# Kernel optimization log

Hardware: AMD Instinct MI355X
Metric: run time of the kernel (lower is better)

Reference implementation:

```python
import jax, jax.numpy as jnp
import numpy as np

EPS = 1e-5
K = 3
N_TAP = K * K


def _bn(x, g, b, m, v):
    # eval-mode batchnorm over channel axis 1 of NCHW
    inv = g / jnp.sqrt(v + EPS)
    return x * inv[None, :, None, None] + (b - m * inv)[None, :, None, None]


def _silu(x):
    return x * jax.nn.sigmoid(x)


def _dcn(x, offset, mask, w, b, pad=1):
    """Modulated deformable conv (DCNv2), stride 1.
    x: [B,C,H,W], offset: [B,2n,H,W] ((dy,dx) per tap), mask: [B,n,H,W],
    w: [O,C,K,K], b: [O]."""
    B, C, H, W = x.shape
    O = w.shape[0]
    ky, kx = jnp.meshgrid(jnp.arange(K), jnp.arange(K), indexing='ij')
    ky = ky.reshape(N_TAP).astype(x.dtype)
    kx = kx.reshape(N_TAP).astype(x.dtype)
    off = offset.reshape(B, N_TAP, 2, H, W)
    base_y = jnp.arange(H, dtype=x.dtype)[None, None, :, None]
    base_x = jnp.arange(W, dtype=x.dtype)[None, None, None, :]
    # fractional sample positions [B,n,H,W]
    py = base_y - pad + ky[None, :, None, None] + off[:, :, 0]
    px = base_x - pad + kx[None, :, None, None] + off[:, :, 1]
    y0 = jnp.floor(py)
    x0 = jnp.floor(px)
    fy = py - y0
    fx = px - x0
    y0i = y0.astype(jnp.int32)
    x0i = x0.astype(jnp.int32)
    x_flat = x.reshape(B, C, 1, H * W)

    def corner(yi, xi, wgt):
        valid = (yi >= 0) & (yi < H) & (xi >= 0) & (xi < W)
        idx = (jnp.clip(yi, 0, H - 1) * W + jnp.clip(xi, 0, W - 1)).reshape(B, 1, N_TAP, H * W)
        v = jnp.take_along_axis(x_flat, idx, axis=-1)  # [B,C,n,HW]
        return v * (wgt * valid.astype(x.dtype)).reshape(B, 1, N_TAP, H * W)

    acc = corner(y0i, x0i, (1 - fy) * (1 - fx))
    acc = acc + corner(y0i, x0i + 1, (1 - fy) * fx)
    acc = acc + corner(y0i + 1, x0i, fy * (1 - fx))
    acc = acc + corner(y0i + 1, x0i + 1, fy * fx)
    val = acc.reshape(B, C, N_TAP, H, W) * mask[:, None]  # modulation
    out = jnp.einsum('bcnhw,ocn->bohw', val, w.reshape(O, C, N_TAP))
    return out + b[None, :, None, None]


def setup_inputs() -> dict:
    key = jax.random.key(0)
    ks = jax.random.split(key, 16)
    B, C1, H, W = 8, 256, 80, 80
    C2 = 256
    Ch = 128  # c_ = int(c2 * 0.5)
    d = {}
    d['x'] = jax.random.normal(ks[0], (B, C1, H, W), jnp.float32)
    # cv1: 1x1 conv (no bias) + BN
    d['cv1_w'] = jax.random.normal(ks[1], (Ch, C1), jnp.float32) * (1.0 / np.sqrt(C1))
    d['bn1_g'] = jax.random.uniform(ks[2], (Ch,), jnp.float32, 0.5, 1.5)
    d['bn1_b'] = jax.random.normal(ks[3], (Ch,), jnp.float32) * 0.1
    d['bn1_m'] = jax.random.normal(ks[4], (Ch,), jnp.float32) * 0.1
    d['bn1_v'] = jax.random.uniform(ks[5], (Ch,), jnp.float32, 0.5, 1.5)
    # offset/mask predictor 3x3 conv (small weights -> modest deformation)
    d['off_w'] = jax.random.normal(ks[6], (3 * N_TAP, Ch, K, K), jnp.float32) * 0.01
    d['off_b'] = jnp.zeros((3 * N_TAP,), jnp.float32)
    # dcn main weight/bias
    d['dcn_w'] = jax.random.normal(ks[7], (Ch, Ch, K, K), jnp.float32) * (1.0 / np.sqrt(Ch * N_TAP))
    d['dcn_b'] = jnp.zeros((Ch,), jnp.float32)
    d['bn2_g'] = jax.random.uniform(ks[8], (Ch,), jnp.float32, 0.5, 1.5)
    d['bn2_b'] = jax.random.normal(ks[9], (Ch,), jnp.float32) * 0.1
    d['bn2_m'] = jax.random.normal(ks[10], (Ch,), jnp.float32) * 0.1
    d['bn2_v'] = jax.random.uniform(ks[11], (Ch,), jnp.float32, 0.5, 1.5)
    # cv2: 1x1 conv (no bias) + BN
    d['cv2_w'] = jax.random.normal(ks[12], (C2, Ch), jnp.float32) * (1.0 / np.sqrt(Ch))
    d['bn3_g'] = jax.random.uniform(ks[13], (C2,), jnp.float32, 0.5, 1.5)
    d['bn3_b'] = jax.random.normal(ks[14], (C2,), jnp.float32) * 0.1
    d['bn3_m'] = jax.random.normal(ks[15], (C2,), jnp.float32) * 0.1
    d['bn3_v'] = jnp.ones((C2,), jnp.float32)
    return d


def reference(x, cv1_w, bn1_g, bn1_b, bn1_m, bn1_v,
              off_w, off_b, dcn_w, dcn_b, bn2_g, bn2_b, bn2_m, bn2_v,
              cv2_w, bn3_g, bn3_b, bn3_m, bn3_v):
    # cv1: 1x1 conv -> BN -> SiLU
    y = _silu(_bn(jnp.einsum('bchw,oc->bohw', x, cv1_w), bn1_g, bn1_b, bn1_m, bn1_v))
    # offset/mask predictor: 3x3 conv, pad 1
    raw = jax.lax.conv_general_dilated(
        y, off_w, window_strides=(1, 1), padding=((1, 1), (1, 1)),
        dimension_numbers=('NCHW', 'OIHW', 'NCHW')) + off_b[None, :, None, None]
    offset = raw[:, :2 * N_TAP]
    mask = jax.nn.sigmoid(raw[:, 2 * N_TAP:])
    # modulated deformable 3x3 conv -> BN -> SiLU
    y = _silu(_bn(_dcn(y, offset, mask, dcn_w, dcn_b), bn2_g, bn2_b, bn2_m, bn2_v))
    # cv2: 1x1 conv -> BN -> SiLU
    y = _silu(_bn(jnp.einsum('bchw,oc->bohw', y, cv2_w), bn3_g, bn3_b, bn3_m, bn3_v))
    return x + y  # shortcut (c1 == c2)
```

## Files before the change

### kernel.cpp

```cpp
#include <hip/hip_runtime.h>
#include <math.h>

#define HWSZ 6400
#define WIMG 80
#define HIMG 80
#define BEPS 1e-5f

typedef __attribute__((ext_vector_type(8))) short short8;
typedef __attribute__((ext_vector_type(4))) float f32x4;

__device__ __forceinline__ unsigned short f2b(float f) {
    unsigned u = __builtin_bit_cast(unsigned, f);
    u += 0x7fffu + ((u >> 16) & 1u);
    return (unsigned short)(u >> 16);
}
__device__ __forceinline__ float b2f(unsigned short h) {
    unsigned u = ((unsigned)h) << 16;
    return __builtin_bit_cast(float, u);
}
__device__ __forceinline__ float silu_f(float t) { return t / (1.f + __expf(-t)); }

#define BPOS(sub, nt, n16, q) (((((sub)*4 + (nt))*16 + (n16))*40) + (q)*8)

__global__ __launch_bounds__(256) void k_prep(
    const float* __restrict__ cv1w, const float* __restrict__ g1, const float* __restrict__ b1,
    const float* __restrict__ m1, const float* __restrict__ v1,
    const float* __restrict__ offw, const float* __restrict__ offb,
    const float* __restrict__ dcnw, const float* __restrict__ dcnb,
    const float* __restrict__ g2, const float* __restrict__ b2,
    const float* __restrict__ m2, const float* __restrict__ v2,
    const float* __restrict__ cv2w, const float* __restrict__ g3, const float* __restrict__ b3,
    const float* __restrict__ m3, const float* __restrict__ v3,
    unsigned short* __restrict__ apk1, unsigned short* __restrict__ apko,
    unsigned short* __restrict__ apkd, unsigned short* __restrict__ apk2,
    float* __restrict__ bias1, float* __restrict__ biaso,
    float* __restrict__ bias2, float* __restrict__ bias3)
{
    int idx = blockIdx.x * 256 + threadIdx.x;
    if (idx < 32768) {
        int j = idx & 7, L = (idx >> 3) & 63, ks = (idx >> 9) & 7, mt = idx >> 12;
        int o = mt * 16 + (L & 15), k = ks * 32 + (L >> 4) * 8 + j;
        float inv = g1[o] * rsqrtf(v1[o] + BEPS);
        apk1[idx] = f2b(cv1w[o * 256 + k] * inv);
    } else if (idx < 69632) {
        int t = idx - 32768;
        int j = t & 7, L = (t >> 3) & 63;
        int mt = t / 18432, rem = t % 18432, ks = rem >> 9;
        int o = mt * 16 + (L & 15);
        int kp = ks * 32 + (L >> 4) * 8 + j;
        int n = kp >> 7, c = kp & 127;
        float wv = (o < 27) ? offw[(size_t)(o * 128 + c) * 9 + n] : 0.f;
        apko[t] = f2b(wv);
    } else if (idx < 217088) {
        int t = idx - 69632;
        int j = t & 7, L = (t >> 3) & 63;
        int mt = t / 18432, rem = t % 18432, ks = rem >> 9;
        int o = mt * 16 + (L & 15);
        int kp = ks * 32 + (L >> 4) * 8 + j;
        int n = kp >> 7, c = kp & 127;
        float inv = g2[o] * rsqrtf(v2[o] + BEPS);
        apkd[t] = f2b(dcnw[(size_t)(o * 128 + c) * 9 + n] * inv);
    } else if (idx < 249856) {
        int t = idx - 217088;
        int j = t & 7, L = (t >> 3) & 63, ks = (t >> 9) & 3, mt = t >> 11;
        int o = mt * 16 + (L & 15), k = ks * 32 + (L >> 4) * 8 + j;
        float inv = g3[o] * rsqrtf(v3[o] + BEPS);
        apk2[t] = f2b(cv2w[o * 128 + k] * inv);
    } else if (idx < 250395) {
        int t = idx - 249856;
        if (t < 128) { float inv = g1[t] * rsqrtf(v1[t] + BEPS); bias1[t] = b1[t] - m1[t] * inv; }
        else if (t < 155) { biaso[t - 128] = offb[t - 128]; }
        else if (t < 283) { int o = t - 155; float inv = g2[o] * rsqrtf(v2[o] + BEPS);
                            bias2[o] = dcnb[o] * inv + b2[o] - m2[o] * inv; }
        else { int o = t - 283; float inv = g3[o] * rsqrtf(v3[o] + BEPS); bias3[o] = b3[o] - m3[o] * inv; }
    }
}

__global__ __launch_bounds__(256) void k_cv1(
    const float* __restrict__ x, const unsigned short* __restrict__ apk1,
    const float* __restrict__ bias1, unsigned short* __restrict__ y1t)
{
    __shared__ __align__(16) unsigned short sB[20480];
    int blk = blockIdx.x;
    int b = blk / 100, pt = blk % 100;
    int p0 = pt * 64;
    int tid = threadIdx.x;
    int lane = tid & 63;
    int w = tid >> 6;
    {
        int px = lane, q = w;
        const float* xb = x + (size_t)b * 256 * HWSZ + p0 + px;
        for (int ks = 0; ks < 8; ++ks) {
            short8 v;
#pragma unroll
            for (int j = 0; j < 8; ++j)
                v[j] = (short)f2b(xb[(size_t)(ks * 32 + q * 8 + j) * HWSZ]);
            *(short8*)&sB[((ks * 4 + (px >> 4)) * 16 + (px & 15)) * 40 + q * 8] = v;
        }
    }
    __syncthreads();
    int n16 = lane & 15, qd = lane >> 4;
    f32x4 acc[2][4];
#pragma unroll
    for (int mi = 0; mi < 2; ++mi)
#pragma unroll
        for (int nt = 0; nt < 4; ++nt) acc[mi][nt] = (f32x4){0.f, 0.f, 0.f, 0.f};
    for (int ks = 0; ks < 8; ++ks) {
        short8 bf[4];
#pragma unroll
        for (int nt = 0; nt < 4; ++nt)
            bf[nt] = *(const short8*)&sB[((ks * 4 + nt) * 16 + n16) * 40 + qd * 8];
#pragma unroll
        for (int mi = 0; mi < 2; ++mi) {
            int mt = w * 2 + mi;
            short8 af = *(const short8*)&apk1[(size_t)((mt * 8 + ks) * 64 + lane) * 8];
#pragma unroll
            for (int nt = 0; nt < 4; ++nt)
                acc[mi][nt] = __builtin_amdgcn_mfma_f32_16x16x32_bf16(af, bf[nt], acc[mi][nt], 0, 0, 0);
        }
    }
    __syncthreads();
#pragma unroll
    for (int mi = 0; mi < 2; ++mi)
#pragma unroll
        for (int nt = 0; nt < 4; ++nt)
#pragma unroll
            for (int r = 0; r < 4; ++r) {
                int o = w * 32 + mi * 16 + qd * 4 + r;
                float sv = silu_f(acc[mi][nt][r] + bias1[o]);
                sB[(nt * 16 + n16) * 136 + o] = f2b(sv);
            }
    __syncthreads();
    {
        int px = tid >> 2, qq = tid & 3;
        unsigned short* ytb = y1t + ((size_t)b * HWSZ + p0 + px) * 128;
#pragma unroll
        for (int seg = 0; seg < 4; ++seg) {
            short8 v = *(const short8*)&sB[px * 136 + qq * 32 + seg * 8];
            *(short8*)&ytb[qq * 32 + seg * 8] = v;
        }
    }
}

__global__ __launch_bounds__(256) void k_off(
    const unsigned short* __restrict__ y1t, const unsigned short* __restrict__ apko,
    const float* __restrict__ biaso, float* __restrict__ raw)
{
    __shared__ __align__(16) unsigned short sV[10240];
    int blk = blockIdx.x;
    int b = blk / 100, pt = blk % 100;
    int p0 = pt * 64;
    int tid = threadIdx.x;
    int lane = tid & 63, w = tid >> 6;
    int n16 = lane & 15, qd = lane >> 4;
    int pxl = tid >> 2, q = tid & 3;
    int p = p0 + pxl;
    int h = p / WIMG, wx = p % WIMG;
    const unsigned short* yb = y1t + (size_t)b * HWSZ * 128;
    f32x4 acc[2];
    acc[0] = (f32x4){0.f, 0.f, 0.f, 0.f};
    acc[1] = (f32x4){0.f, 0.f, 0.f, 0.f};
    const short8 zz = {0, 0, 0, 0, 0, 0, 0, 0};
    for (int n = 0; n < 9; ++n) {
        int hh = h - 1 + n / 3, ww = wx - 1 + n % 3;
        bool valid = ((unsigned)hh < HIMG) && ((unsigned)ww < WIMG);
        int spx = valid ? hh * WIMG + ww : 0;
        const unsigned short* ys = yb + (size_t)spx * 128 + q * 8;
#pragma unroll
        for (int sub = 0; sub < 4; ++sub) {
            short8 v = *(const short8*)&ys[sub * 32];
            if (!valid) v = zz;
            *(short8*)&sV[BPOS(sub, pxl >> 4, pxl & 15, q)] = v;
        }
        __syncthreads();
#pragma unroll
        for (int sub = 0; sub < 4; ++sub) {
            int ks = n * 4 + sub;
            short8 bf = *(const short8*)&sV[BPOS(sub, w, n16, qd)];
#pragma unroll
            for (int mi = 0; mi < 2; ++mi) {
                short8 af = *(const short8*)&apko[(size_t)((mi * 36 + ks) * 64 + lane) * 8];
                acc[mi] = __builtin_amdgcn_mfma_f32_16x16x32_bf16(af, bf, acc[mi], 0, 0, 0);
            }
        }
        __syncthreads();
    }
    float* rb = raw + (size_t)b * 27 * HWSZ + p0 + w * 16 + n16;
#pragma unroll
    for (int mi = 0; mi < 2; ++mi)
#pragma unroll
        for (int r = 0; r < 4; ++r) {
            int o = mi * 16 + qd * 4 + r;
            if (o < 27) {
                float t = acc[mi][r] + biaso[o];
                if (o >= 18) t = 1.f / (1.f + __expf(-t));
                rb[(size_t)o * HWSZ] = t;
            }
        }
}

__global__ __launch_bounds__(256) void k_dcn(
    const unsigned short* __restrict__ y1t, const float* __restrict__ raw,
    const unsigned short* __restrict__ apkd, const float* __restrict__ bias2,
    unsigned short* __restrict__ zt)
{
    __shared__ float swgt[4][9][64];
    __shared__ unsigned short sidx[4][9][64];
    __shared__ __align__(16) unsigned short sV[10240];
    int blk = blockIdx.x;
    int b = blk / 100, pt = blk % 100;
    int p0 = pt * 64;
    int tid = threadIdx.x;

    for (int i = tid; i < 576; i += 256) {
        int n = i / 64, pp = i % 64;
        int p = p0 + pp;
        int h = p / WIMG, wx = p % WIMG;
        const float* rb = raw + (size_t)b * 27 * HWSZ + p;
        float dy = rb[(size_t)(2 * n) * HWSZ];
        float dx = rb[(size_t)(2 * n + 1) * HWSZ];
        float mk = rb[(size_t)(18 + n) * HWSZ];
        float py = (float)(h - 1 + n / 3) + dy;
        float px = (float)(wx - 1 + n % 3) + dx;
        float y0f = floorf(py), x0f = floorf(px);
        float fy = py - y0f, fx = px - x0f;
        int y0 = (int)y0f, x0 = (int)x0f;
#pragma unroll
        for (int k = 0; k < 4; ++k) {
            int yy = y0 + (k >> 1);
            int xx = x0 + (k & 1);
            bool valid = ((unsigned)yy < HIMG) && ((unsigned)xx < WIMG);
            float wk = ((k >> 1) ? fy : 1.f - fy) * ((k & 1) ? fx : 1.f - fx);
            wk = valid ? wk * mk : 0.f;
            int yc = min(max(yy, 0), HIMG - 1);
            int xc = min(max(xx, 0), WIMG - 1);
            sidx[k][n][pp] = (unsigned short)(yc * WIMG + xc);
            swgt[k][n][pp] = wk;
        }
    }
    __syncthreads();

    int lane = tid & 63, w = tid >> 6;
    int n16 = lane & 15, qd = lane >> 4;
    int pxl = tid >> 2, q = tid & 3;
    const unsigned short* yb = y1t + (size_t)b * HWSZ * 128;
    f32x4 acc[2][4];
#pragma unroll
    for (int mi = 0; mi < 2; ++mi)
#pragma unroll
        for (int nt = 0; nt < 4; ++nt) acc[mi][nt] = (f32x4){0.f, 0.f, 0.f, 0.f};

    for (int n = 0; n < 9; ++n) {
        float av[4][8];
#pragma unroll
        for (int sub = 0; sub < 4; ++sub)
#pragma unroll
            for (int j = 0; j < 8; ++j) av[sub][j] = 0.f;
#pragma unroll
        for (int k = 0; k < 4; ++k) {
            float wk = swgt[k][n][pxl];
            const unsigned short* ys = yb + (size_t)sidx[k][n][pxl] * 128 + q * 8;
#pragma unroll
            for (int sub = 0; sub < 4; ++sub) {
                short8 v = *(const short8*)&ys[sub * 32];
#pragma unroll
                for (int j = 0; j < 8; ++j)
                    av[sub][j] = fmaf(wk, b2f((unsigned short)v[j]), av[sub][j]);
            }
        }
#pragma unroll
        for (int sub = 0; sub < 4; ++sub) {
            short8 v;
#pragma unroll
            for (int j = 0; j < 8; ++j) v[j] = (short)f2b(av[sub][j]);
            *(short8*)&sV[BPOS(sub, pxl >> 4, pxl & 15, q)] = v;
        }
        __syncthreads();
#pragma unroll
        for (int sub = 0; sub < 4; ++sub) {
            int ks = n * 4 + sub;
            short8 bf[4];
#pragma unroll
            for (int nt = 0; nt < 4; ++nt)
                bf[nt] = *(const short8*)&sV[BPOS(sub, nt, n16, qd)];
#pragma unroll
            for (int mi = 0; mi < 2; ++mi) {
                short8 af = *(const short8*)&apkd[(size_t)(((2 * w + mi) * 36 + ks) * 64 + lane) * 8];
#pragma unroll
                for (int nt = 0; nt < 4; ++nt)
                    acc[mi][nt] = __builtin_amdgcn_mfma_f32_16x16x32_bf16(af, bf[nt], acc[mi][nt], 0, 0, 0);
            }
        }
        __syncthreads();
    }
#pragma unroll
    for (int mi = 0; mi < 2; ++mi)
#pragma unroll
        for (int nt = 0; nt < 4; ++nt)
#pragma unroll
            for (int r = 0; r < 4; ++r) {
                int o = w * 32 + mi * 16 + qd * 4 + r;
                float sv = silu_f(acc[mi][nt][r] + bias2[o]);
                sV[(nt * 16 + n16) * 136 + o] = f2b(sv);
            }
    __syncthreads();
    {
        int px = tid >> 2, qq = tid & 3;
        unsigned short* zb = zt + ((size_t)b * HWSZ + p0 + px) * 128;
#pragma unroll
        for (int seg = 0; seg < 4; ++seg) {
            short8 v = *(const short8*)&sV[px * 136 + qq * 32 + seg * 8];
            *(short8*)&zb[qq * 32 + seg * 8] = v;
        }
    }
}

__global__ __launch_bounds__(256) void k_cv2(
    const unsigned short* __restrict__ zt, const float* __restrict__ x,
    const unsigned short* __restrict__ apk2, const float* __restrict__ bias3,
    float* __restrict__ out)
{
    int blk = blockIdx.x;
    int b = blk / 100, pt = blk % 100;
    int p0 = pt * 64;
    int tid = threadIdx.x;
    int lane = tid & 63, w = tid >> 6;
    int n16 = lane & 15, qd = lane >> 4;
    const unsigned short* zb = zt + ((size_t)b * HWSZ + p0) * 128;
    f32x4 acc[4][4];
#pragma unroll
    for (int mi = 0; mi < 4; ++mi)
#pragma unroll
        for (int nt = 0; nt < 4; ++nt) acc[mi][nt] = (f32x4){0.f, 0.f, 0.f, 0.f};
#pragma unroll
    for (int ks = 0; ks < 4; ++ks) {
        short8 bf[4];
#pragma unroll
        for (int nt = 0; nt < 4; ++nt)
            bf[nt] = *(const short8*)&zb[(size_t)(nt * 16 + n16) * 128 + ks * 32 + qd * 8];
#pragma unroll
        for (int mi = 0; mi < 4; ++mi) {
            int mt = w * 4 + mi;
            short8 af = *(const short8*)&apk2[(size_t)((mt * 4 + ks) * 64 + lane) * 8];
#pragma unroll
            for (int nt = 0; nt < 4; ++nt)
                acc[mi][nt] = __builtin_amdgcn_mfma_f32_16x16x32_bf16(af, bf[nt], acc[mi][nt], 0, 0, 0);
        }
    }
    const float* xb = x + (size_t)b * 256 * HWSZ;
    float* ob = out + (size_t)b * 256 * HWSZ;
#pragma unroll
    for (int mi = 0; mi < 4; ++mi)
#pragma unroll
        for (int nt = 0; nt < 4; ++nt)
#pragma unroll
            for (int r = 0; r < 4; ++r) {
                int o = w * 64 + mi * 16 + qd * 4 + r;
                size_t idx = (size_t)o * HWSZ + p0 + nt * 16 + n16;
                ob[idx] = xb[idx] + silu_f(acc[mi][nt][r] + bias3[o]);
            }
}

extern "C" void kernel_launch(void* const* d_in, const int* in_sizes, int n_in,
                              void* d_out, int out_size, void* d_ws, size_t ws_size,
                              hipStream_t stream) {
    const float* x     = (const float*)d_in[0];
    const float* cv1w  = (const float*)d_in[1];
    const float* bn1g  = (const float*)d_in[2];
    const float* bn1b  = (const float*)d_in[3];
    const float* bn1m  = (const float*)d_in[4];
    const float* bn1v  = (const float*)d_in[5];
    const float* offw  = (const float*)d_in[6];
    const float* offb  = (const float*)d_in[7];
    const float* dcnw  = (const float*)d_in[8];
    const float* dcnb  = (const float*)d_in[9];
    const float* bn2g  = (const float*)d_in[10];
    const float* bn2b  = (const float*)d_in[11];
    const float* bn2m  = (const float*)d_in[12];
    const float* bn2v  = (const float*)d_in[13];
    const float* cv2w  = (const float*)d_in[14];
    const float* bn3g  = (const float*)d_in[15];
    const float* bn3b  = (const float*)d_in[16];
    const float* bn3m  = (const float*)d_in[17];
    const float* bn3v  = (const float*)d_in[18];
    float* out = (float*)d_out;

    float* base = (float*)d_ws;
    unsigned short* y1t = (unsigned short*)base;
    float* raw   = base + 3276800;
    unsigned short* zt  = (unsigned short*)(base + 4659200);
    unsigned short* apk1 = (unsigned short*)(base + 7936000);
    unsigned short* apko = (unsigned short*)(base + 7952384);
    unsigned short* apkd = (unsigned short*)(base + 7970816);
    unsigned short* apk2 = (unsigned short*)(base + 8044544);
    float* bias1 = base + 8060928;
    float* biaso = base + 8061056;
    float* bias2 = base + 8061088;
    float* bias3 = base + 8061216;

    k_prep<<<979, 256, 0, stream>>>(cv1w, bn1g, bn1b, bn1m, bn1v,
                                    offw, offb, dcnw, dcnb,
                                    bn2g, bn2b, bn2m, bn2v,
                                    cv2w, bn3g, bn3b, bn3m, bn3v,
                                    apk1, apko, apkd, apk2,
                                    bias1, biaso, bias2, bias3);
    k_cv1<<<800, 256, 0, stream>>>(x, apk1, bias1, y1t);
    k_off<<<800, 256, 0, stream>>>(y1t, apko, biaso, raw);
    k_dcn<<<800, 256, 0, stream>>>(y1t, raw, apkd, bias2, zt);
    k_cv2<<<800, 256, 0, stream>>>(zt, x, apk2, bias3, out);
}
```

Measured before the change: 234.3 us.

## Fuse offset conv into DCN kernel and drop LDS staging of B operands

Merges the offset/mask predictor kernel into the deformable conv kernel, so the raw offsets live in shared memory instead of a global round trip. It also restructures cv1 and dcn so each wave owns 16 pixels and all 128 output channels, and builds MFMA B operands directly in registers rather than staging them through LDS with barriers. Outputs are written straight from the accumulators as 4-short vectors, and the block index is remapped to interleave batches. The price is 8 accumulator tiles per wave (more registers), repeated A-weight loads per wave, and smaller, less coalesced stores.

```diff
diff --git a/kernel.cpp b/kernel.cpp
--- a/kernel.cpp
+++ b/kernel.cpp
@@ -7,6 +7,7 @@
 #define BEPS 1e-5f
 
 typedef __attribute__((ext_vector_type(8))) short short8;
+typedef __attribute__((ext_vector_type(4))) short s16x4;
 typedef __attribute__((ext_vector_type(4))) float f32x4;
 
 __device__ __forceinline__ unsigned short f2b(float f) {
@@ -19,8 +20,6 @@
     return __builtin_bit_cast(float, u);
 }
 __device__ __forceinline__ float silu_f(float t) { return t / (1.f + __expf(-t)); }
-
-#define BPOS(sub, nt, n16, q) (((((sub)*4 + (nt))*16 + (n16))*40) + (q)*8)
 
 __global__ __launch_bounds__(256) void k_prep(
     const float* __restrict__ cv1w, const float* __restrict__ g1, const float* __restrict__ b1,
@@ -80,148 +79,104 @@
     const float* __restrict__ x, const unsigned short* __restrict__ apk1,
     const float* __restrict__ bias1, unsigned short* __restrict__ y1t)
 {
-    __shared__ __align__(16) unsigned short sB[20480];
     int blk = blockIdx.x;
-    int b = blk / 100, pt = blk % 100;
-    int p0 = pt * 64;
-    int tid = threadIdx.x;
-    int lane = tid & 63;
-    int w = tid >> 6;
-    {
-        int px = lane, q = w;
-        const float* xb = x + (size_t)b * 256 * HWSZ + p0 + px;
-        for (int ks = 0; ks < 8; ++ks) {
-            short8 v;
-#pragma unroll
-            for (int j = 0; j < 8; ++j)
-                v[j] = (short)f2b(xb[(size_t)(ks * 32 + q * 8 + j) * HWSZ]);
-            *(short8*)&sB[((ks * 4 + (px >> 4)) * 16 + (px & 15)) * 40 + q * 8] = v;
-        }
-    }
-    __syncthreads();
-    int n16 = lane & 15, qd = lane >> 4;
-    f32x4 acc[2][4];
-#pragma unroll
-    for (int mi = 0; mi < 2; ++mi)
-#pragma unroll
-        for (int nt = 0; nt < 4; ++nt) acc[mi][nt] = (f32x4){0.f, 0.f, 0.f, 0.f};
-    for (int ks = 0; ks < 8; ++ks) {
-        short8 bf[4];
-#pragma unroll
-        for (int nt = 0; nt < 4; ++nt)
-            bf[nt] = *(const short8*)&sB[((ks * 4 + nt) * 16 + n16) * 40 + qd * 8];
-#pragma unroll
-        for (int mi = 0; mi < 2; ++mi) {
-            int mt = w * 2 + mi;
-            short8 af = *(const short8*)&apk1[(size_t)((mt * 8 + ks) * 64 + lane) * 8];
-#pragma unroll
-            for (int nt = 0; nt < 4; ++nt)
-                acc[mi][nt] = __builtin_amdgcn_mfma_f32_16x16x32_bf16(af, bf[nt], acc[mi][nt], 0, 0, 0);
-        }
-    }
-    __syncthreads();
-#pragma unroll
-    for (int mi = 0; mi < 2; ++mi)
-#pragma unroll
-        for (int nt = 0; nt < 4; ++nt)
-#pragma unroll
-            for (int r = 0; r < 4; ++r) {
-                int o = w * 32 + mi * 16 + qd * 4 + r;
-                float sv = silu_f(acc[mi][nt][r] + bias1[o]);
-                sB[(nt * 16 + n16) * 136 + o] = f2b(sv);
-            }
-    __syncthreads();
-    {
-        int px = tid >> 2, qq = tid & 3;
-        unsigned short* ytb = y1t + ((size_t)b * HWSZ + p0 + px) * 128;
-#pragma unroll
-        for (int seg = 0; seg < 4; ++seg) {
-            short8 v = *(const short8*)&sB[px * 136 + qq * 32 + seg * 8];
-            *(short8*)&ytb[qq * 32 + seg * 8] = v;
-        }
-    }
-}
-
-__global__ __launch_bounds__(256) void k_off(
-    const unsigned short* __restrict__ y1t, const unsigned short* __restrict__ apko,
-    const float* __restrict__ biaso, float* __restrict__ raw)
-{
-    __shared__ __align__(16) unsigned short sV[10240];
-    int blk = blockIdx.x;
-    int b = blk / 100, pt = blk % 100;
+    int b = blk & 7, pt = blk >> 3;
     int p0 = pt * 64;
     int tid = threadIdx.x;
     int lane = tid & 63, w = tid >> 6;
     int n16 = lane & 15, qd = lane >> 4;
-    int pxl = tid >> 2, q = tid & 3;
+    int px = p0 + w * 16 + n16;
+    const float* xb = x + (size_t)b * 256 * HWSZ + px;
+    f32x4 acc[8];
+#pragma unroll
+    for (int mt = 0; mt < 8; ++mt) acc[mt] = (f32x4){0.f, 0.f, 0.f, 0.f};
+#pragma unroll 2
+    for (int ks = 0; ks < 8; ++ks) {
+        short8 bf;
+#pragma unroll
+        for (int j = 0; j < 8; ++j)
+            bf[j] = (short)f2b(xb[(size_t)(ks * 32 + qd * 8 + j) * HWSZ]);
+#pragma unroll
+        for (int mt = 0; mt < 8; ++mt) {
+            short8 af = *(const short8*)&apk1[(size_t)((mt * 8 + ks) * 64 + lane) * 8];
+            acc[mt] = __builtin_amdgcn_mfma_f32_16x16x32_bf16(af, bf, acc[mt], 0, 0, 0);
+        }
+    }
+    unsigned short* ytb = y1t + ((size_t)b * HWSZ + px) * 128;
+#pragma unroll
+    for (int mt = 0; mt < 8; ++mt) {
+        int o0 = mt * 16 + qd * 4;
+        s16x4 v;
+#pragma unroll
+        for (int r = 0; r < 4; ++r)
+            v[r] = (short)f2b(silu_f(acc[mt][r] + bias1[o0 + r]));
+        *(s16x4*)&ytb[o0] = v;
+    }
+}
+
+__global__ __launch_bounds__(256) void k_dcn(
+    const unsigned short* __restrict__ y1t,
+    const unsigned short* __restrict__ apko, const float* __restrict__ biaso,
+    const unsigned short* __restrict__ apkd, const float* __restrict__ bias2,
+    unsigned short* __restrict__ zt)
+{
+    __shared__ float rawL[27 * 66];
+    __shared__ float swgt[4][9][64];
+    __shared__ unsigned short sidx[4][9][64];
+    int blk = blockIdx.x;
+    int b = blk & 7, pt = blk >> 3;
+    int p0 = pt * 64;
+    int tid = threadIdx.x;
+    int lane = tid & 63, w = tid >> 6;
+    int n16 = lane & 15, qd = lane >> 4;
+    int pxl = w * 16 + n16;
     int p = p0 + pxl;
     int h = p / WIMG, wx = p % WIMG;
     const unsigned short* yb = y1t + (size_t)b * HWSZ * 128;
-    f32x4 acc[2];
-    acc[0] = (f32x4){0.f, 0.f, 0.f, 0.f};
-    acc[1] = (f32x4){0.f, 0.f, 0.f, 0.f};
+
+    f32x4 oacc[2];
+    oacc[0] = (f32x4){0.f, 0.f, 0.f, 0.f};
+    oacc[1] = (f32x4){0.f, 0.f, 0.f, 0.f};
     const short8 zz = {0, 0, 0, 0, 0, 0, 0, 0};
     for (int n = 0; n < 9; ++n) {
         int hh = h - 1 + n / 3, ww = wx - 1 + n % 3;
         bool valid = ((unsigned)hh < HIMG) && ((unsigned)ww < WIMG);
         int spx = valid ? hh * WIMG + ww : 0;
-        const unsigned short* ys = yb + (size_t)spx * 128 + q * 8;
+        const unsigned short* ys = yb + (size_t)spx * 128 + qd * 8;
 #pragma unroll
         for (int sub = 0; sub < 4; ++sub) {
             short8 v = *(const short8*)&ys[sub * 32];
             if (!valid) v = zz;
-            *(short8*)&sV[BPOS(sub, pxl >> 4, pxl & 15, q)] = v;
-        }
-        __syncthreads();
-#pragma unroll
-        for (int sub = 0; sub < 4; ++sub) {
             int ks = n * 4 + sub;
-            short8 bf = *(const short8*)&sV[BPOS(sub, w, n16, qd)];
 #pragma unroll
             for (int mi = 0; mi < 2; ++mi) {
                 short8 af = *(const short8*)&apko[(size_t)((mi * 36 + ks) * 64 + lane) * 8];
-                acc[mi] = __builtin_amdgcn_mfma_f32_16x16x32_bf16(af, bf, acc[mi], 0, 0, 0);
-            }
-        }
-        __syncthreads();
-    }
-    float* rb = raw + (size_t)b * 27 * HWSZ + p0 + w * 16 + n16;
+                oacc[mi] = __builtin_amdgcn_mfma_f32_16x16x32_bf16(af, v, oacc[mi], 0, 0, 0);
+            }
+        }
+    }
 #pragma unroll
     for (int mi = 0; mi < 2; ++mi)
 #pragma unroll
         for (int r = 0; r < 4; ++r) {
             int o = mi * 16 + qd * 4 + r;
             if (o < 27) {
-                float t = acc[mi][r] + biaso[o];
+                float t = oacc[mi][r] + biaso[o];
                 if (o >= 18) t = 1.f / (1.f + __expf(-t));
-                rb[(size_t)o * HWSZ] = t;
-            }
-        }
-}
-
-__global__ __launch_bounds__(256) void k_dcn(
-    const unsigned short* __restrict__ y1t, const float* __restrict__ raw,
-    const unsigned short* __restrict__ apkd, const float* __restrict__ bias2,
-    unsigned short* __restrict__ zt)
-{
-    __shared__ float swgt[4][9][64];
-    __shared__ unsigned short sidx[4][9][64];
-    __shared__ __align__(16) unsigned short sV[10240];
-    int blk = blockIdx.x;
-    int b = blk / 100, pt = blk % 100;
-    int p0 = pt * 64;
-    int tid = threadIdx.x;
+                rawL[o * 66 + pxl] = t;
+            }
+        }
+    __syncthreads();
 
     for (int i = tid; i < 576; i += 256) {
-        int n = i / 64, pp = i % 64;
-        int p = p0 + pp;
-        int h = p / WIMG, wx = p % WIMG;
-        const float* rb = raw + (size_t)b * 27 * HWSZ + p;
-        float dy = rb[(size_t)(2 * n) * HWSZ];
-        float dx = rb[(size_t)(2 * n + 1) * HWSZ];
-        float mk = rb[(size_t)(18 + n) * HWSZ];
-        float py = (float)(h - 1 + n / 3) + dy;
-        float px = (float)(wx - 1 + n % 3) + dx;
+        int n = i >> 6, pp = i & 63;
+        int pg = p0 + pp;
+        int hg = pg / WIMG, wg = pg % WIMG;
+        float dy = rawL[(2 * n) * 66 + pp];
+        float dx = rawL[(2 * n + 1) * 66 + pp];
+        float mk = rawL[(18 + n) * 66 + pp];
+        float py = (float)(hg - 1 + n / 3) + dy;
+        float px = (float)(wg - 1 + n % 3) + dx;
         float y0f = floorf(py), x0f = floorf(px);
         float fy = py - y0f, fx = px - x0f;
         int y0 = (int)y0f, x0 = (int)x0f;
@@ -240,16 +195,9 @@
     }
     __syncthreads();
 
-    int lane = tid & 63, w = tid >> 6;
-    int n16 = lane & 15, qd = lane >> 4;
-    int pxl = tid >> 2, q = tid & 3;
-    const unsigned short* yb = y1t + (size_t)b * HWSZ * 128;
-    f32x4 acc[2][4];
-#pragma unroll
-    for (int mi = 0; mi < 2; ++mi)
-#pragma unroll
-        for (int nt = 0; nt < 4; ++nt) acc[mi][nt] = (f32x4){0.f, 0.f, 0.f, 0.f};
-
+    f32x4 acc[8];
+#pragma unroll
+    for (int mt = 0; mt < 8; ++mt) acc[mt] = (f32x4){0.f, 0.f, 0.f, 0.f};
     for (int n = 0; n < 9; ++n) {
         float av[4][8];
 #pragma unroll
@@ -259,7 +207,7 @@
 #pragma unroll
         for (int k = 0; k < 4; ++k) {
             float wk = swgt[k][n][pxl];
-            const unsigned short* ys = yb + (size_t)sidx[k][n][pxl] * 128 + q * 8;
+            const unsigned short* ys = yb + (size_t)sidx[k][n][pxl] * 128 + qd * 8;
 #pragma unroll
             for (int sub = 0; sub < 4; ++sub) {
                 short8 v = *(const short8*)&ys[sub * 32];
@@ -270,48 +218,26 @@
         }
 #pragma unroll
         for (int sub = 0; sub < 4; ++sub) {
-            short8 v;
-#pragma unroll
-            for (int j = 0; j < 8; ++j) v[j] = (short)f2b(av[sub][j]);
-            *(short8*)&sV[BPOS(sub, pxl >> 4, pxl & 15, q)] = v;
-        }
-        __syncthreads();
-#pragma unroll
-        for (int sub = 0; sub < 4; ++sub) {
+            short8 bfv;
+#pragma unroll
+            for (int j = 0; j < 8; ++j) bfv[j] = (short)f2b(av[sub][j]);
             int ks = n * 4 + sub;
-            short8 bf[4];
-#pragma unroll
-            for (int nt = 0; nt < 4; ++nt)
-                bf[nt] = *(const short8*)&sV[BPOS(sub, nt, n16, qd)];
-#pragma unroll
-            for (int mi = 0; mi < 2; ++mi) {
-                short8 af = *(const short8*)&apkd[(size_t)(((2 * w + mi) * 36 + ks) * 64 + lane) * 8];
-#pragma unroll
-                for (int nt = 0; nt < 4; ++nt)
-                    acc[mi][nt] = __builtin_amdgcn_mfma_f32_16x16x32_bf16(af, bf[nt], acc[mi][nt], 0, 0, 0);
-            }
-        }
-        __syncthreads();
-    }
-#pragma unroll
-    for (int mi = 0; mi < 2; ++mi)
-#pragma unroll
-        for (int nt = 0; nt < 4; ++nt)
-#pragma unroll
-            for (int r = 0; r < 4; ++r) {
-                int o = w * 32 + mi * 16 + qd * 4 + r;
-                float sv = silu_f(acc[mi][nt][r] + bias2[o]);
-                sV[(nt * 16 + n16) * 136 + o] = f2b(sv);
-            }
-    __syncthreads();
-    {
-        int px = tid >> 2, qq = tid & 3;
-        unsigned short* zb = zt + ((size_t)b * HWSZ + p0 + px) * 128;
-#pragma unroll
-        for (int seg = 0; seg < 4; ++seg) {
-            short8 v = *(const short8*)&sV[px * 136 + qq * 32 + seg * 8];
-            *(short8*)&zb[qq * 32 + seg * 8] = v;
-        }
+#pragma unroll
+            for (int mt = 0; mt < 8; ++mt) {
+                short8 af = *(const short8*)&apkd[(size_t)((mt * 36 + ks) * 64 + lane) * 8];
+                acc[mt] = __builtin_amdgcn_mfma_f32_16x16x32_bf16(af, bfv, acc[mt], 0, 0, 0);
+            }
+        }
+    }
+    unsigned short* zb = zt + ((size_t)b * HWSZ + p) * 128;
+#pragma unroll
+    for (int mt = 0; mt < 8; ++mt) {
+        int o0 = mt * 16 + qd * 4;
+        s16x4 v;
+#pragma unroll
+        for (int r = 0; r < 4; ++r)
+            v[r] = (short)f2b(silu_f(acc[mt][r] + bias2[o0 + r]));
+        *(s16x4*)&zb[o0] = v;
     }
 }
 
@@ -321,7 +247,7 @@
     float* __restrict__ out)
 {
     int blk = blockIdx.x;
-    int b = blk / 100, pt = blk % 100;
+    int b = blk & 7, pt = blk >> 3;
     int p0 = pt * 64;
     int tid = threadIdx.x;
     int lane = tid & 63, w = tid >> 6;
@@ -387,16 +313,15 @@
 
     float* base = (float*)d_ws;
     unsigned short* y1t = (unsigned short*)base;
-    float* raw   = base + 3276800;
-    unsigned short* zt  = (unsigned short*)(base + 4659200);
-    unsigned short* apk1 = (unsigned short*)(base + 7936000);
-    unsigned short* apko = (unsigned short*)(base + 7952384);
-    unsigned short* apkd = (unsigned short*)(base + 7970816);
-    unsigned short* apk2 = (unsigned short*)(base + 8044544);
-    float* bias1 = base + 8060928;
-    float* biaso = base + 8061056;
-    float* bias2 = base + 8061088;
-    float* bias3 = base + 8061216;
+    unsigned short* zt  = (unsigned short*)(base + 3276800);
+    unsigned short* apk1 = (unsigned short*)(base + 6553600);
+    unsigned short* apko = (unsigned short*)(base + 6569984);
+    unsigned short* apkd = (unsigned short*)(base + 6588416);
+    unsigned short* apk2 = (unsigned short*)(base + 6662144);
+    float* bias1 = base + 6678528;
+    float* biaso = base + 6678656;
+    float* bias2 = base + 6678688;
+    float* bias3 = base + 6678816;
 
     k_prep<<<979, 256, 0, stream>>>(cv1w, bn1g, bn1b, bn1m, bn1v,
                                     offw, offb, dcnw, dcnb,
@@ -405,7 +330,6 @@
                                     apk1, apko, apkd, apk2,
                                     bias1, biaso, bias2, bias3);
     k_cv1<<<800, 256, 0, stream>>>(x, apk1, bias1, y1t);
-    k_off<<<800, 256, 0, stream>>>(y1t, apko, biaso, raw);
-    k_dcn<<<800, 256, 0, stream>>>(y1t, raw, apkd, bias2, zt);
+    k_dcn<<<800, 256, 0, stream>>>(y1t, apko, biaso, apkd, bias2, zt);
     k_cv2<<<800, 256, 0, stream>>>(zt, x, apk2, bias3, out);
 }
```

Result: slower. 355.4 us (+51.6%).

## Drop LDS staging in cv1/dcn epilogues and interleave batch in block mapping

Applied to the files above, without the earlier changes.

k_cv1 no longer stages the input tile through shared memory. Each wave converts its own 16-pixel column of x to bf16 in registers and computes all 8 output tiles, then writes SiLU outputs directly with 8-byte stores. The k_dcn epilogue likewise skips the LDS transpose and its barrier, storing 4-channel vectors straight to global memory. All kernels now map blocks batch-fastest (blk&7), so adjacent blocks touch the same spatial tile across batches. The cost is narrower, more scattered global stores and more weight (A-fragment) loads per wave in cv1.

```diff
diff --git a/kernel.cpp b/kernel.cpp
--- a/kernel.cpp
+++ b/kernel.cpp
@@ -7,6 +7,7 @@
 #define BEPS 1e-5f
 
 typedef __attribute__((ext_vector_type(8))) short short8;
+typedef __attribute__((ext_vector_type(4))) short s16x4;
 typedef __attribute__((ext_vector_type(4))) float f32x4;
 
 __device__ __forceinline__ unsigned short f2b(float f) {
@@ -80,65 +81,38 @@
     const float* __restrict__ x, const unsigned short* __restrict__ apk1,
     const float* __restrict__ bias1, unsigned short* __restrict__ y1t)
 {
-    __shared__ __align__(16) unsigned short sB[20480];
     int blk = blockIdx.x;
-    int b = blk / 100, pt = blk % 100;
+    int b = blk & 7, pt = blk >> 3;
     int p0 = pt * 64;
     int tid = threadIdx.x;
-    int lane = tid & 63;
-    int w = tid >> 6;
-    {
-        int px = lane, q = w;
-        const float* xb = x + (size_t)b * 256 * HWSZ + p0 + px;
-        for (int ks = 0; ks < 8; ++ks) {
-            short8 v;
-#pragma unroll
-            for (int j = 0; j < 8; ++j)
-                v[j] = (short)f2b(xb[(size_t)(ks * 32 + q * 8 + j) * HWSZ]);
-            *(short8*)&sB[((ks * 4 + (px >> 4)) * 16 + (px & 15)) * 40 + q * 8] = v;
-        }
-    }
-    __syncthreads();
+    int lane = tid & 63, w = tid >> 6;
     int n16 = lane & 15, qd = lane >> 4;
-    f32x4 acc[2][4];
-#pragma unroll
-    for (int mi = 0; mi < 2; ++mi)
-#pragma unroll
-        for (int nt = 0; nt < 4; ++nt) acc[mi][nt] = (f32x4){0.f, 0.f, 0.f, 0.f};
+    int px = p0 + w * 16 + n16;
+    const float* xb = x + (size_t)b * 256 * HWSZ + px;
+    f32x4 acc[8];
+#pragma unroll
+    for (int mt = 0; mt < 8; ++mt) acc[mt] = (f32x4){0.f, 0.f, 0.f, 0.f};
+#pragma unroll 2
     for (int ks = 0; ks < 8; ++ks) {
-        short8 bf[4];
-#pragma unroll
-        for (int nt = 0; nt < 4; ++nt)
-            bf[nt] = *(const short8*)&sB[((ks * 4 + nt) * 16 + n16) * 40 + qd * 8];
-#pragma unroll
-        for (int mi = 0; mi < 2; ++mi) {
-            int mt = w * 2 + mi;
+        short8 bf;
+#pragma unroll
+        for (int j = 0; j < 8; ++j)
+            bf[j] = (short)f2b(xb[(size_t)(ks * 32 + qd * 8 + j) * HWSZ]);
+#pragma unroll
+        for (int mt = 0; mt < 8; ++mt) {
             short8 af = *(const short8*)&apk1[(size_t)((mt * 8 + ks) * 64 + lane) * 8];
-#pragma unroll
-            for (int nt = 0; nt < 4; ++nt)
-                acc[mi][nt] = __builtin_amdgcn_mfma_f32_16x16x32_bf16(af, bf[nt], acc[mi][nt], 0, 0, 0);
-        }
-    }
-    __syncthreads();
-#pragma unroll
-    for (int mi = 0; mi < 2; ++mi)
-#pragma unroll
-        for (int nt = 0; nt < 4; ++nt)
-#pragma unroll
-            for (int r = 0; r < 4; ++r) {
-                int o = w * 32 + mi * 16 + qd * 4 + r;
-                float sv = silu_f(acc[mi][nt][r] + bias1[o]);
-                sB[(nt * 16 + n16) * 136 + o] = f2b(sv);
-            }
-    __syncthreads();
-    {
-        int px = tid >> 2, qq = tid & 3;
-        unsigned short* ytb = y1t + ((size_t)b * HWSZ + p0 + px) * 128;
-#pragma unroll
-        for (int seg = 0; seg < 4; ++seg) {
-            short8 v = *(const short8*)&sB[px * 136 + qq * 32 + seg * 8];
-            *(short8*)&ytb[qq * 32 + seg * 8] = v;
-        }
+            acc[mt] = __builtin_amdgcn_mfma_f32_16x16x32_bf16(af, bf, acc[mt], 0, 0, 0);
+        }
+    }
+    unsigned short* ytb = y1t + ((size_t)b * HWSZ + px) * 128;
+#pragma unroll
+    for (int mt = 0; mt < 8; ++mt) {
+        int o0 = mt * 16 + qd * 4;
+        s16x4 v;
+#pragma unroll
+        for (int r = 0; r < 4; ++r)
+            v[r] = (short)f2b(silu_f(acc[mt][r] + bias1[o0 + r]));
+        *(s16x4*)&ytb[o0] = v;
     }
 }
 
@@ -148,7 +122,7 @@
 {
     __shared__ __align__(16) unsigned short sV[10240];
     int blk = blockIdx.x;
-    int b = blk / 100, pt = blk % 100;
+    int b = blk & 7, pt = blk >> 3;
     int p0 = pt * 64;
     int tid = threadIdx.x;
     int lane = tid & 63, w = tid >> 6;
@@ -208,7 +182,7 @@
     __shared__ unsigned short sidx[4][9][64];
     __shared__ __align__(16) unsigned short sV[10240];
     int blk = blockIdx.x;
-    int b = blk / 100, pt = blk % 100;
+    int b = blk & 7, pt = blk >> 3;
     int p0 = pt * 64;
     int tid = threadIdx.x;
 
@@ -293,26 +267,19 @@
         }
         __syncthreads();
     }
+    unsigned short* zb = zt + ((size_t)b * HWSZ + p0) * 128;
 #pragma unroll
     for (int mi = 0; mi < 2; ++mi)
 #pragma unroll
-        for (int nt = 0; nt < 4; ++nt)
-#pragma unroll
-            for (int r = 0; r < 4; ++r) {
-                int o = w * 32 + mi * 16 + qd * 4 + r;
-                float sv = silu_f(acc[mi][nt][r] + bias2[o]);
-                sV[(nt * 16 + n16) * 136 + o] = f2b(sv);
-            }
-    __syncthreads();
-    {
-        int px = tid >> 2, qq = tid & 3;
-        unsigned short* zb = zt + ((size_t)b * HWSZ + p0 + px) * 128;
-#pragma unroll
-        for (int seg = 0; seg < 4; ++seg) {
-            short8 v = *(const short8*)&sV[px * 136 + qq * 32 + seg * 8];
-            *(short8*)&zb[qq * 32 + seg * 8] = v;
-        }
-    }
+        for (int nt = 0; nt < 4; ++nt) {
+            int o0 = (2 * w + mi) * 16 + qd * 4;
+            int px = nt * 16 + n16;
+            s16x4 v;
+#pragma unroll
+            for (int r = 0; r < 4; ++r)
+                v[r] = (short)f2b(silu_f(acc[mi][nt][r] + bias2[o0 + r]));
+            *(s16x4*)&zb[(size_t)px * 128 + o0] = v;
+        }
 }
 
 __global__ __launch_bounds__(256) void k_cv2(
@@ -321,7 +288,7 @@
     float* __restrict__ out)
 {
     int blk = blockIdx.x;
-    int b = blk / 100, pt = blk % 100;
+    int b = blk & 7, pt = blk >> 3;
     int p0 = pt * 64;
     int tid = threadIdx.x;
     int lane = tid & 63, w = tid >> 6;
```

Measured after the change: 260.3 us. 1.11x slower.
